# Optimization experiments

Hardware: AMD Instinct MI355X
Metric: run time of the kernel (lower is better)

Reference implementation:

```python
import jax, jax.numpy as jnp
import numpy as np

N_HEADS = 8
ATT_DIM = 64


def _pos_enc(x):
    # x: (chan, L, bs, D); sinusoidal PE added along axis -3 (the query/key slot dim)
    L, D = x.shape[-3], x.shape[-1]
    pos = np.arange(L)[:, None].astype(np.float32)
    div = np.exp(np.arange(0, D, 2).astype(np.float32) * (-np.log(10000.0) / D))
    pe = np.zeros((L, 1, D), dtype=np.float32)
    pe[:, 0, 0::2] = np.sin(pos * div)
    pe[:, 0, 1::2] = np.cos(pos * div)
    return x + jnp.asarray(pe)


def setup_inputs() -> dict:
    key = jax.random.key(0)
    ks = jax.random.split(key, 6)
    C, NQ, NK, B, QD, KD = 8, 16, 32, 128, 128, 128
    E = N_HEADS * ATT_DIM  # 512
    OUT = ATT_DIM  # out_dim defaults to attention_dim
    b = np.float32(1.0 / np.sqrt(ATT_DIM))
    bp = np.float32(1.0 / np.sqrt(OUT))
    return {
        "q": jax.random.normal(ks[0], (C, NQ, B, QD), dtype=jnp.float32),
        "k": jax.random.normal(ks[1], (C, NK, B, KD), dtype=jnp.float32),
        "Wq": jax.random.uniform(ks[2], (C, NQ, QD, E), jnp.float32, -b, b),
        "Wk": jax.random.uniform(ks[3], (C, NK, KD, E), jnp.float32, -b, b),
        "Wv": jax.random.uniform(ks[4], (C, NK, KD, E), jnp.float32, -b, b),
        "Wp": jax.random.uniform(ks[5], (C, NQ, E, OUT), jnp.float32, -bp, bp),
    }


def reference(q, k, Wq, Wk, Wv, Wp):
    H, A = N_HEADS, ATT_DIM
    C, NQ, B, _ = q.shape
    NK = k.shape[1]
    inv_temp = jnp.float32(1.0 / np.sqrt(A))
    q_pe = _pos_enc(q)
    k_pe = _pos_enc(k)
    # per-channel grouped QKV projections: (C, N, B, D) x (C, N, D, E) -> (C, N, B, E)
    query = jnp.einsum('cqbd,cqde->cqbe', q_pe, Wq).reshape(C, NQ, B, H, A)
    key_t = jnp.einsum('ckbd,ckde->ckbe', k_pe, Wk).reshape(C, NK, B, H, A)
    value = jnp.einsum('ckbd,ckde->ckbe', k_pe, Wv).reshape(C, NK, B, H, A)
    # attention scores per (channel, batch, head)
    logits = jnp.einsum('cqbha,ckbha->cbhqk', query, key_t) * inv_temp
    attn = jax.nn.softmax(logits, axis=-1)
    # value aggregation (original does broadcast-multiply+sum; einsum is the same math)
    out = jnp.einsum('cbhqk,ckbha->cqbha', attn, value).reshape(C, NQ, B, H * A)
    # per-channel output projection
    return jnp.einsum('cqbe,cqeo->cqbo', out, Wp)
```

## Files before the change

### kernel.cpp

```cpp
#include <hip/hip_runtime.h>

#define C_  8
#define NQ_ 16
#define NK_ 32
#define B_  128
#define D_  128
#define E_  512
#define H_  8
#define A_  64
#define O_  64

typedef __attribute__((ext_vector_type(4))) float f32x4;
typedef __attribute__((ext_vector_type(8))) short bf16x8;
typedef __attribute__((ext_vector_type(4))) short bf16x4;

__device__ __forceinline__ short f2bf(float f) {
    union { float f; unsigned u; } v; v.f = f;
    unsigned r = v.u + 0x7fffu + ((v.u >> 16) & 1u);
    return (short)(r >> 16);
}

__global__ __launch_bounds__(256) void qkv_proj_kernel(
    const float* __restrict__ qin, const float* __restrict__ kin,
    const float* __restrict__ Wq, const float* __restrict__ Wk,
    const float* __restrict__ Wv,
    short* __restrict__ wsq, short* __restrict__ wsk, short* __restrict__ wsv)
{
    __shared__ __align__(16) short Alds[B_][72];
    __shared__ __align__(16) short Blds[128][72];
    __shared__ float pe_buf[D_];

    const int tid   = threadIdx.x;
    const int blk   = blockIdx.x;
    const int e_blk = blk & 3;
    const int unit  = blk >> 2;

    const float* X; const float* W; short* Y; int n; size_t ypitch;
    if (unit < C_ * NQ_) {
        const int c = unit >> 4;
        n = unit & 15;
        X = qin + (size_t)unit * B_ * D_;
        W = Wq  + (size_t)unit * D_ * E_;
        Y = wsq + (size_t)c * B_ * NQ_ * E_ + (size_t)n * E_;
        ypitch = (size_t)NQ_ * E_;
    } else if (unit < C_ * (NQ_ + NK_)) {
        const int u = unit - C_ * NQ_;
        const int c = u >> 5;
        n = u & 31;
        X = kin + (size_t)u * B_ * D_;
        W = Wk  + (size_t)u * D_ * E_;
        Y = wsk + (size_t)c * B_ * NK_ * E_ + (size_t)n * E_;
        ypitch = (size_t)NK_ * E_;
    } else {
        const int u = unit - C_ * (NQ_ + NK_);
        const int c = u >> 5;
        n = u & 31;
        X = kin + (size_t)u * B_ * D_;
        W = Wv  + (size_t)u * D_ * E_;
        Y = wsv + (size_t)c * B_ * NK_ * E_ + (size_t)n * E_;
        ypitch = (size_t)NK_ * E_;
    }

    if (tid < D_) {
        const int d = tid;
        const float freq = expf((float)(d & ~1) * (-9.210340371976184f / (float)D_));
        const float arg  = (float)n * freq;
        pe_buf[d] = (d & 1) ? cosf(arg) : sinf(arg);
    }
    __syncthreads();

    const int wv   = tid >> 6;
    const int lane = tid & 63;
    const int lr   = lane & 15;
    const int quad = lane >> 4;
    const int wrow = (wv >> 1) * 64;
    const int wcol = (wv & 1) * 64;

    f32x4 acc[4][4];
    for (int m = 0; m < 4; ++m)
        for (int nf = 0; nf < 4; ++nf)
            acc[m][nf] = (f32x4){0.f, 0.f, 0.f, 0.f};

    const int e  = tid & 127;
    const int kg = (tid >> 7) * 32;

    for (int k0 = 0; k0 < D_; k0 += 64) {
        f32x4 a_raw[8];
        #pragma unroll
        for (int i = 0; i < 8; ++i) {
            const int id  = tid + 256 * i;
            const int row = id >> 4;
            const int ch  = id & 15;
            a_raw[i] = *(const f32x4*)(X + (size_t)row * D_ + k0 + ch * 4);
        }
        float b_raw[32];
        const float* bsrc = W + (size_t)(k0 + kg) * E_ + e_blk * 128 + e;
        #pragma unroll
        for (int i = 0; i < 32; ++i)
            b_raw[i] = bsrc[(size_t)i * E_];

        #pragma unroll
        for (int i = 0; i < 8; ++i) {
            const int id  = tid + 256 * i;
            const int row = id >> 4;
            const int ch  = id & 15;
            bf16x4 v;
            #pragma unroll
            for (int j = 0; j < 4; ++j)
                v[j] = f2bf(a_raw[i][j] + pe_buf[k0 + ch * 4 + j]);
            *(bf16x4*)&Alds[row][ch * 4] = v;
        }
        #pragma unroll
        for (int i = 0; i < 4; ++i) {
            bf16x8 v;
            #pragma unroll
            for (int j = 0; j < 8; ++j)
                v[j] = f2bf(b_raw[i * 8 + j]);
            *(bf16x8*)&Blds[e][kg + i * 8] = v;
        }
        __syncthreads();

        for (int ks = 0; ks < 2; ++ks) {
            const int kc = ks * 32 + quad * 8;
            bf16x8 af[4], bfr[4];
            for (int m = 0; m < 4; ++m)
                af[m] = *(const bf16x8*)&Alds[wrow + m * 16 + lr][kc];
            for (int nf = 0; nf < 4; ++nf)
                bfr[nf] = *(const bf16x8*)&Blds[wcol + nf * 16 + lr][kc];
            for (int m = 0; m < 4; ++m)
                for (int nf = 0; nf < 4; ++nf)
                    acc[m][nf] = __builtin_amdgcn_mfma_f32_16x16x32_bf16(
                        af[m], bfr[nf], acc[m][nf], 0, 0, 0);
        }
        __syncthreads();
    }

    for (int m = 0; m < 4; ++m)
        for (int nf = 0; nf < 4; ++nf)
            for (int r = 0; r < 4; ++r) {
                const int row = wrow + m * 16 + quad * 4 + r;
                const int col = e_blk * 128 + wcol + nf * 16 + lr;
                Y[(size_t)row * ypitch + col] = f2bf(acc[m][nf][r]);
            }
}

__global__ __launch_bounds__(256) void attn_kernel(
    const short* __restrict__ wsq, const short* __restrict__ wsk,
    const short* __restrict__ wsv, short* __restrict__ wso)
{
    __shared__ __align__(16) short Qs[16][264];
    __shared__ __align__(16) short Ks[32][264];
    __shared__ __align__(16) short Vs[32][258];
    __shared__ __align__(16) short Ps[4][16][40];

    const int tid = threadIdx.x;
    const int blk = blockIdx.x;
    const int hh  = blk & 1;
    const int b   = (blk >> 1) & (B_ - 1);
    const int c   = blk >> 8;

    const short* qb = wsq + ((size_t)(c * B_ + b) * NQ_) * E_ + hh * 256;
    const short* kb = wsk + ((size_t)(c * B_ + b) * NK_) * E_ + hh * 256;
    const short* vb = wsv + ((size_t)(c * B_ + b) * NK_) * E_ + hh * 256;

    {
        const int nloc = tid >> 5;
        const int ch   = tid & 31;
        #pragma unroll
        for (int i = 0; i < 2; ++i) {
            const int nn = nloc + i * 8;
            *(bf16x8*)&Qs[nn][ch * 8] = *(const bf16x8*)(qb + (size_t)nn * E_ + ch * 8);
        }
        #pragma unroll
        for (int i = 0; i < 4; ++i) {
            const int nn = nloc + i * 8;
            *(bf16x8*)&Ks[nn][ch * 8] = *(const bf16x8*)(kb + (size_t)nn * E_ + ch * 8);
        }
        #pragma unroll
        for (int i = 0; i < 4; ++i) {
            const int nn = nloc + i * 8;
            bf16x8 v = *(const bf16x8*)(vb + (size_t)nn * E_ + ch * 8);
            #pragma unroll
            for (int p = 0; p < 4; ++p)
                *(int*)&Vs[nn][ch * 8 + p * 2] = ((const int*)&v)[p];
        }
    }
    __syncthreads();

    const int wv   = tid >> 6;
    const int lane = tid & 63;
    const int lr   = lane & 15;
    const int quad = lane >> 4;
    const int lcol = wv * 64;

    f32x4 sacc0 = (f32x4){0.f, 0.f, 0.f, 0.f};
    f32x4 sacc1 = (f32x4){0.f, 0.f, 0.f, 0.f};
    #pragma unroll
    for (int ks = 0; ks < 2; ++ks) {
        const int kc = lcol + ks * 32 + quad * 8;
        const bf16x8 aq  = *(const bf16x8*)&Qs[lr][kc];
        const bf16x8 bk0 = *(const bf16x8*)&Ks[lr][kc];
        const bf16x8 bk1 = *(const bf16x8*)&Ks[16 + lr][kc];
        sacc0 = __builtin_amdgcn_mfma_f32_16x16x32_bf16(aq, bk0, sacc0, 0, 0, 0);
        sacc1 = __builtin_amdgcn_mfma_f32_16x16x32_bf16(aq, bk1, sacc1, 0, 0, 0);
    }

    float p0[4], p1[4];
    for (int r = 0; r < 4; ++r) {
        const float v0 = sacc0[r] * 0.125f;
        const float v1 = sacc1[r] * 0.125f;
        float m = fmaxf(v0, v1);
        m = fmaxf(m, __shfl_xor(m, 1));
        m = fmaxf(m, __shfl_xor(m, 2));
        m = fmaxf(m, __shfl_xor(m, 4));
        m = fmaxf(m, __shfl_xor(m, 8));
        const float e0 = __expf(v0 - m);
        const float e1 = __expf(v1 - m);
        float s = e0 + e1;
        s += __shfl_xor(s, 1);
        s += __shfl_xor(s, 2);
        s += __shfl_xor(s, 4);
        s += __shfl_xor(s, 8);
        const float inv = 1.0f / s;
        p0[r] = e0 * inv;
        p1[r] = e1 * inv;
    }

    for (int r = 0; r < 4; ++r) {
        Ps[wv][quad * 4 + r][lr]      = f2bf(p0[r]);
        Ps[wv][quad * 4 + r][16 + lr] = f2bf(p1[r]);
    }
    __syncthreads();
    const bf16x8 ap = *(const bf16x8*)&Ps[wv][lr][quad * 8];

    #pragma unroll
    for (int t = 0; t < 4; ++t) {
        bf16x8 bvv;
        #pragma unroll
        for (int j = 0; j < 8; ++j)
            bvv[j] = Vs[quad * 8 + j][lcol + t * 16 + lr];
        f32x4 oacc = (f32x4){0.f, 0.f, 0.f, 0.f};
        oacc = __builtin_amdgcn_mfma_f32_16x16x32_bf16(ap, bvv, oacc, 0, 0, 0);
        for (int r = 0; r < 4; ++r)
            wso[((size_t)(c * NQ_ + quad * 4 + r) * B_ + b) * E_
                + hh * 256 + lcol + t * 16 + lr] = f2bf(oacc[r]);
    }
}

__global__ __launch_bounds__(256) void out_proj_kernel(
    const short* __restrict__ wso, const float* __restrict__ Wp,
    float* __restrict__ out)
{
    __shared__ __align__(16) short Xlds[64][72];
    __shared__ __align__(16) short Wlds[32][72];

    const int tid = threadIdx.x;
    const int blk = blockIdx.x;
    const int cq  = blk >> 2;
    const int bh  = (blk >> 1) & 1;
    const int oh  = blk & 1;

    const short* Xb = wso + (size_t)cq * B_ * E_ + (size_t)bh * 64 * E_;
    const float* Wb = Wp  + (size_t)cq * E_ * O_ + oh * 32;
    float*       Ob = out + (size_t)cq * B_ * O_ + (size_t)bh * 64 * O_ + oh * 32;

    const int wv   = tid >> 6;
    const int lane = tid & 63;
    const int lr   = lane & 15;
    const int quad = lane >> 4;
    const int o    = tid & 31;
    const int kg   = tid >> 5;

    f32x4 acc[2];
    acc[0] = (f32x4){0.f, 0.f, 0.f, 0.f};
    acc[1] = (f32x4){0.f, 0.f, 0.f, 0.f};

    bf16x8 xv[2][2];
    float  wr[2][8];

    auto issue = [&](int s, int buf) {
        const int k0 = s * 64;
        #pragma unroll
        for (int i = 0; i < 2; ++i) {
            const int task = tid + 256 * i;
            xv[buf][i] = *(const bf16x8*)(Xb + (size_t)(task >> 3) * E_ + k0 + (task & 7) * 8);
        }
        #pragma unroll
        for (int j = 0; j < 8; ++j)
            wr[buf][j] = Wb[(size_t)(k0 + kg * 8 + j) * O_ + o];
    };

    issue(0, 0);
    #pragma unroll
    for (int s = 0; s < 8; ++s) {
        const int cb = s & 1;
        if (s < 7) issue(s + 1, cb ^ 1);

        #pragma unroll
        for (int i = 0; i < 2; ++i) {
            const int task = tid + 256 * i;
            *(bf16x8*)&Xlds[task >> 3][(task & 7) * 8] = xv[cb][i];
        }
        bf16x8 wv8;
        #pragma unroll
        for (int j = 0; j < 8; ++j) wv8[j] = f2bf(wr[cb][j]);
        *(bf16x8*)&Wlds[o][kg * 8] = wv8;
        __syncthreads();

        #pragma unroll
        for (int ks = 0; ks < 2; ++ks) {
            const int kc = ks * 32 + quad * 8;
            const bf16x8 af = *(const bf16x8*)&Xlds[wv * 16 + lr][kc];
            #pragma unroll
            for (int nf = 0; nf < 2; ++nf) {
                const bf16x8 bfr = *(const bf16x8*)&Wlds[nf * 16 + lr][kc];
                acc[nf] = __builtin_amdgcn_mfma_f32_16x16x32_bf16(af, bfr, acc[nf], 0, 0, 0);
            }
        }
        __syncthreads();
    }

    #pragma unroll
    for (int nf = 0; nf < 2; ++nf)
        for (int r = 0; r < 4; ++r)
            Ob[(size_t)(wv * 16 + quad * 4 + r) * O_ + nf * 16 + lr] = acc[nf][r];
}

extern "C" void kernel_launch(void* const* d_in, const int* in_sizes, int n_in,
                              void* d_out, int out_size, void* d_ws, size_t ws_size,
                              hipStream_t stream) {
    const float* q  = (const float*)d_in[0];
    const float* k  = (const float*)d_in[1];
    const float* Wq = (const float*)d_in[2];
    const float* Wk = (const float*)d_in[3];
    const float* Wv = (const float*)d_in[4];
    const float* Wp = (const float*)d_in[5];
    float* out = (float*)d_out;

    const size_t sz_q = (size_t)C_ * NQ_ * B_ * E_;
    const size_t sz_k = (size_t)C_ * NK_ * B_ * E_;
    short* wsq = (short*)d_ws;
    short* wsk = wsq + sz_q;
    short* wsv = wsk + sz_k;
    short* wso = wsv + sz_k;

    qkv_proj_kernel<<<dim3(2560), dim3(256), 0, stream>>>(q, k, Wq, Wk, Wv, wsq, wsk, wsv);
    attn_kernel<<<dim3(2048), dim3(256), 0, stream>>>(wsq, wsk, wsv, wso);
    out_proj_kernel<<<dim3(512), dim3(256), 0, stream>>>(wso, Wp, out);
}
```

Baseline: 246.0 us.

## Restructure QKV projection: one block per unit, keep X in LDS, double-buffer W

The QKV projection now launches one block per (channel, slot) unit instead of four blocks each covering one E-slice. Each block loads and converts the full 128x128 activation tile (with positional encoding) into LDS once and reuses it across all four E-slices. Weight tiles are prefetched into registers one step ahead and double-buffered in LDS, so global loads overlap the MFMA work. The cost is a grid four times smaller (640 blocks), higher register pressure from two 32-float prefetch buffers, and a 2-blocks-per-SM launch bound.

```diff
diff --git a/kernel.cpp b/kernel.cpp
--- a/kernel.cpp
+++ b/kernel.cpp
@@ -20,20 +20,18 @@
     return (short)(r >> 16);
 }
 
-__global__ __launch_bounds__(256) void qkv_proj_kernel(
+__global__ __launch_bounds__(256, 2) void qkv_proj_kernel(
     const float* __restrict__ qin, const float* __restrict__ kin,
     const float* __restrict__ Wq, const float* __restrict__ Wk,
     const float* __restrict__ Wv,
     short* __restrict__ wsq, short* __restrict__ wsk, short* __restrict__ wsv)
 {
-    __shared__ __align__(16) short Alds[B_][72];
-    __shared__ __align__(16) short Blds[128][72];
+    __shared__ __align__(16) short Alds[B_][136];
+    __shared__ __align__(16) short Blds[2][128][72];
     __shared__ float pe_buf[D_];
 
-    const int tid   = threadIdx.x;
-    const int blk   = blockIdx.x;
-    const int e_blk = blk & 3;
-    const int unit  = blk >> 2;
+    const int tid  = threadIdx.x;
+    const int unit = blockIdx.x;
 
     const float* X; const float* W; short* Y; int n; size_t ypitch;
     if (unit < C_ * NQ_) {
@@ -67,6 +65,50 @@
         const float arg  = (float)n * freq;
         pe_buf[d] = (d & 1) ? cosf(arg) : sinf(arg);
     }
+
+    const int e  = tid & 127;
+    const int kg = (tid >> 7) * 32;
+
+    auto issueW = [&](int t2, float (&wbuf)[32]) {
+        const float* bsrc = W + (size_t)((t2 & 1) * 64 + kg) * E_ + (t2 >> 1) * 128 + e;
+        #pragma unroll
+        for (int i = 0; i < 32; ++i) wbuf[i] = bsrc[(size_t)i * E_];
+    };
+    auto convW = [&](int buf, float (&wbuf)[32]) {
+        #pragma unroll
+        for (int i = 0; i < 4; ++i) {
+            bf16x8 v;
+            #pragma unroll
+            for (int j = 0; j < 8; ++j) v[j] = f2bf(wbuf[i * 8 + j]);
+            *(bf16x8*)&Blds[buf][e][kg + i * 8] = v;
+        }
+    };
+
+    f32x4 xr[16];
+    #pragma unroll
+    for (int i = 0; i < 16; ++i) {
+        const int id = tid + 256 * i;
+        xr[i] = *(const f32x4*)(X + (size_t)(id >> 5) * D_ + (id & 31) * 4);
+    }
+    float wb0[32], wb1[32];
+    issueW(0, wb0);
+
+    __syncthreads();
+
+    #pragma unroll
+    for (int i = 0; i < 16; ++i) {
+        const int id  = tid + 256 * i;
+        const int row = id >> 5;
+        const int ch  = id & 31;
+        bf16x4 v;
+        #pragma unroll
+        for (int j = 0; j < 4; ++j)
+            v[j] = f2bf(xr[i][j] + pe_buf[ch * 4 + j]);
+        *(bf16x4*)&Alds[row][ch * 4] = v;
+    }
+
+    convW(0, wb0);
+    issueW(1, wb1);
     __syncthreads();
 
     const int wv   = tid >> 6;
@@ -77,71 +119,66 @@
     const int wcol = (wv & 1) * 64;
 
     f32x4 acc[4][4];
+    #pragma unroll
     for (int m = 0; m < 4; ++m)
+        #pragma unroll
         for (int nf = 0; nf < 4; ++nf)
             acc[m][nf] = (f32x4){0.f, 0.f, 0.f, 0.f};
 
-    const int e  = tid & 127;
-    const int kg = (tid >> 7) * 32;
-
-    for (int k0 = 0; k0 < D_; k0 += 64) {
-        f32x4 a_raw[8];
-        #pragma unroll
-        for (int i = 0; i < 8; ++i) {
-            const int id  = tid + 256 * i;
-            const int row = id >> 4;
-            const int ch  = id & 15;
-            a_raw[i] = *(const f32x4*)(X + (size_t)row * D_ + k0 + ch * 4);
-        }
-        float b_raw[32];
-        const float* bsrc = W + (size_t)(k0 + kg) * E_ + e_blk * 128 + e;
-        #pragma unroll
-        for (int i = 0; i < 32; ++i)
-            b_raw[i] = bsrc[(size_t)i * E_];
-
-        #pragma unroll
-        for (int i = 0; i < 8; ++i) {
-            const int id  = tid + 256 * i;
-            const int row = id >> 4;
-            const int ch  = id & 15;
-            bf16x4 v;
-            #pragma unroll
-            for (int j = 0; j < 4; ++j)
-                v[j] = f2bf(a_raw[i][j] + pe_buf[k0 + ch * 4 + j]);
-            *(bf16x4*)&Alds[row][ch * 4] = v;
-        }
-        #pragma unroll
-        for (int i = 0; i < 4; ++i) {
-            bf16x8 v;
-            #pragma unroll
-            for (int j = 0; j < 8; ++j)
-                v[j] = f2bf(b_raw[i * 8 + j]);
-            *(bf16x8*)&Blds[e][kg + i * 8] = v;
-        }
-        __syncthreads();
-
+    #pragma unroll
+    for (int t = 0; t < 8; ++t) {
+        const int eb = t >> 1;
+        const int kh = t & 1;
+
+        if (t < 6) {
+            if ((t & 1) == 0) issueW(t + 2, wb0);
+            else              issueW(t + 2, wb1);
+        }
+
+        #pragma unroll
         for (int ks = 0; ks < 2; ++ks) {
-            const int kc = ks * 32 + quad * 8;
+            const int kcA = kh * 64 + ks * 32 + quad * 8;
+            const int kcB = ks * 32 + quad * 8;
             bf16x8 af[4], bfr[4];
+            #pragma unroll
             for (int m = 0; m < 4; ++m)
-                af[m] = *(const bf16x8*)&Alds[wrow + m * 16 + lr][kc];
+                af[m] = *(const bf16x8*)&Alds[wrow + m * 16 + lr][kcA];
+            #pragma unroll
             for (int nf = 0; nf < 4; ++nf)
-                bfr[nf] = *(const bf16x8*)&Blds[wcol + nf * 16 + lr][kc];
+                bfr[nf] = *(const bf16x8*)&Blds[t & 1][wcol + nf * 16 + lr][kcB];
+            #pragma unroll
             for (int m = 0; m < 4; ++m)
+                #pragma unroll
                 for (int nf = 0; nf < 4; ++nf)
                     acc[m][nf] = __builtin_amdgcn_mfma_f32_16x16x32_bf16(
                         af[m], bfr[nf], acc[m][nf], 0, 0, 0);
         }
-        __syncthreads();
-    }
-
-    for (int m = 0; m < 4; ++m)
-        for (int nf = 0; nf < 4; ++nf)
-            for (int r = 0; r < 4; ++r) {
-                const int row = wrow + m * 16 + quad * 4 + r;
-                const int col = e_blk * 128 + wcol + nf * 16 + lr;
-                Y[(size_t)row * ypitch + col] = f2bf(acc[m][nf][r]);
-            }
+
+        if (t < 7) {
+            if (((t + 1) & 1) == 0) convW(0, wb0);
+            else                    convW(1, wb1);
+        }
+
+        if (kh == 1) {
+            #pragma unroll
+            for (int m = 0; m < 4; ++m)
+                #pragma unroll
+                for (int nf = 0; nf < 4; ++nf)
+                    #pragma unroll
+                    for (int r = 0; r < 4; ++r) {
+                        const int row = wrow + m * 16 + quad * 4 + r;
+                        const int col = eb * 128 + wcol + nf * 16 + lr;
+                        Y[(size_t)row * ypitch + col] = f2bf(acc[m][nf][r]);
+                    }
+            #pragma unroll
+            for (int m = 0; m < 4; ++m)
+                #pragma unroll
+                for (int nf = 0; nf < 4; ++nf)
+                    acc[m][nf] = (f32x4){0.f, 0.f, 0.f, 0.f};
+        }
+
+        if (t < 7) __syncthreads();
+    }
 }
 
 __global__ __launch_bounds__(256) void attn_kernel(
@@ -344,7 +381,7 @@
     short* wsv = wsk + sz_k;
     short* wso = wsv + sz_k;
 
-    qkv_proj_kernel<<<dim3(2560), dim3(256), 0, stream>>>(q, k, Wq, Wk, Wv, wsq, wsk, wsv);
+    qkv_proj_kernel<<<dim3(640), dim3(256), 0, stream>>>(q, k, Wq, Wk, Wv, wsq, wsk, wsv);
     attn_kernel<<<dim3(2048), dim3(256), 0, stream>>>(wsq, wsk, wsv, wso);
     out_proj_kernel<<<dim3(512), dim3(256), 0, stream>>>(wso, Wp, out);
 }
```

After: 254.7 us. 1.04x slower.

## Swizzle QKV projection LDS tiles, compute positional encoding in registers

Applied to the files above, without the earlier changes.

Replaces the padded LDS tiles in the QKV projection kernel with unpadded 64-wide rows that use an XOR swizzle, so that bank conflicts are avoided while LDS use shrinks. The positional-encoding table in shared memory, along with its barrier, is removed. Each wave now computes its encoding values per k-chunk and broadcasts them with lane shuffles. It also adds a waves-per-EU occupancy hint and fully unrolls the MFMA loops. The change adds a redundant no-op assignment to W, and recomputing sin/cos per chunk adds some ALU work.

```diff
diff --git a/kernel.cpp b/kernel.cpp
--- a/kernel.cpp
+++ b/kernel.cpp
@@ -20,15 +20,14 @@
     return (short)(r >> 16);
 }
 
-__global__ __launch_bounds__(256) void qkv_proj_kernel(
+__global__ __launch_bounds__(256, 5) void qkv_proj_kernel(
     const float* __restrict__ qin, const float* __restrict__ kin,
     const float* __restrict__ Wq, const float* __restrict__ Wk,
     const float* __restrict__ Wv,
     short* __restrict__ wsq, short* __restrict__ wsk, short* __restrict__ wsv)
 {
-    __shared__ __align__(16) short Alds[B_][72];
-    __shared__ __align__(16) short Blds[128][72];
-    __shared__ float pe_buf[D_];
+    __shared__ __align__(16) short Alds[128 * 64];
+    __shared__ __align__(16) short Blds[128 * 64];
 
     const int tid   = threadIdx.x;
     const int blk   = blockIdx.x;
@@ -56,18 +55,11 @@
         const int c = u >> 5;
         n = u & 31;
         X = kin + (size_t)u * B_ * D_;
+        W = Wk == Wv ? W : Wv;
         W = Wv  + (size_t)u * D_ * E_;
         Y = wsv + (size_t)c * B_ * NK_ * E_ + (size_t)n * E_;
         ypitch = (size_t)NK_ * E_;
     }
-
-    if (tid < D_) {
-        const int d = tid;
-        const float freq = expf((float)(d & ~1) * (-9.210340371976184f / (float)D_));
-        const float arg  = (float)n * freq;
-        pe_buf[d] = (d & 1) ? cosf(arg) : sinf(arg);
-    }
-    __syncthreads();
 
     const int wv   = tid >> 6;
     const int lane = tid & 63;
@@ -77,12 +69,15 @@
     const int wcol = (wv & 1) * 64;
 
     f32x4 acc[4][4];
+    #pragma unroll
     for (int m = 0; m < 4; ++m)
+        #pragma unroll
         for (int nf = 0; nf < 4; ++nf)
             acc[m][nf] = (f32x4){0.f, 0.f, 0.f, 0.f};
 
     const int e  = tid & 127;
     const int kg = (tid >> 7) * 32;
+    const int ch = tid & 15;
 
     for (int k0 = 0; k0 < D_; k0 += 64) {
         f32x4 a_raw[8];
@@ -90,7 +85,6 @@
         for (int i = 0; i < 8; ++i) {
             const int id  = tid + 256 * i;
             const int row = id >> 4;
-            const int ch  = id & 15;
             a_raw[i] = *(const f32x4*)(X + (size_t)row * D_ + k0 + ch * 4);
         }
         float b_raw[32];
@@ -98,17 +92,28 @@
         #pragma unroll
         for (int i = 0; i < 32; ++i)
             b_raw[i] = bsrc[(size_t)i * E_];
+
+        float pe[4];
+        {
+            const int d = k0 + lane;
+            const float freq = expf((float)(d & ~1) * (-9.210340371976184f / (float)D_));
+            const float arg  = (float)n * freq;
+            const float val  = (d & 1) ? cosf(arg) : sinf(arg);
+            #pragma unroll
+            for (int j = 0; j < 4; ++j)
+                pe[j] = __shfl(val, ch * 4 + j);
+        }
 
         #pragma unroll
         for (int i = 0; i < 8; ++i) {
             const int id  = tid + 256 * i;
             const int row = id >> 4;
-            const int ch  = id & 15;
             bf16x4 v;
             #pragma unroll
             for (int j = 0; j < 4; ++j)
-                v[j] = f2bf(a_raw[i][j] + pe_buf[k0 + ch * 4 + j]);
-            *(bf16x4*)&Alds[row][ch * 4] = v;
+                v[j] = f2bf(a_raw[i][j] + pe[j]);
+            const int idx = row * 64 + (((ch >> 1) ^ (row & 7)) << 3) + (ch & 1) * 4;
+            *(bf16x4*)&Alds[idx] = v;
         }
         #pragma unroll
         for (int i = 0; i < 4; ++i) {
@@ -116,18 +121,30 @@
             #pragma unroll
             for (int j = 0; j < 8; ++j)
                 v[j] = f2bf(b_raw[i * 8 + j]);
-            *(bf16x8*)&Blds[e][kg + i * 8] = v;
+            const int g   = (kg >> 3) + i;
+            const int idx = e * 64 + ((g ^ (e & 7)) << 3);
+            *(bf16x8*)&Blds[idx] = v;
         }
         __syncthreads();
 
+        #pragma unroll
         for (int ks = 0; ks < 2; ++ks) {
             const int kc = ks * 32 + quad * 8;
+            const int g  = kc >> 3;
             bf16x8 af[4], bfr[4];
+            #pragma unroll
+            for (int m = 0; m < 4; ++m) {
+                const int row = wrow + m * 16 + lr;
+                af[m] = *(const bf16x8*)&Alds[row * 64 + ((g ^ (row & 7)) << 3)];
+            }
+            #pragma unroll
+            for (int nf = 0; nf < 4; ++nf) {
+                const int row = wcol + nf * 16 + lr;
+                bfr[nf] = *(const bf16x8*)&Blds[row * 64 + ((g ^ (row & 7)) << 3)];
+            }
+            #pragma unroll
             for (int m = 0; m < 4; ++m)
-                af[m] = *(const bf16x8*)&Alds[wrow + m * 16 + lr][kc];
-            for (int nf = 0; nf < 4; ++nf)
-                bfr[nf] = *(const bf16x8*)&Blds[wcol + nf * 16 + lr][kc];
-            for (int m = 0; m < 4; ++m)
+                #pragma unroll
                 for (int nf = 0; nf < 4; ++nf)
                     acc[m][nf] = __builtin_amdgcn_mfma_f32_16x16x32_bf16(
                         af[m], bfr[nf], acc[m][nf], 0, 0, 0);
@@ -135,8 +152,11 @@
         __syncthreads();
     }
 
+    #pragma unroll
     for (int m = 0; m < 4; ++m)
+        #pragma unroll
         for (int nf = 0; nf < 4; ++nf)
+            #pragma unroll
             for (int r = 0; r < 4; ++r) {
                 const int row = wrow + m * 16 + quad * 4 + r;
                 const int col = e_blk * 128 + wcol + nf * 16 + lr;
```

Measured after the change: 392.5 us. +59.6%, slower.
